# Optimization experiments

Hardware: AMD Instinct MI355X
Metric: run time of the kernel (lower is better)

## Reference

```python
import jax, jax.numpy as jnp
import numpy as np

P = 4  # polynomial kernel degree


def setup_inputs() -> dict:
    key = jax.random.key(0)
    k1, k2, k3, k4 = jax.random.split(key, 4)
    m, n, d = 16384, 8192, 64
    x_p = jax.random.normal(k1, (m, d), dtype=jnp.float32)
    X = jax.random.normal(k2, (n, d), dtype=jnp.float32)
    alpha = jax.random.uniform(k3, (n,), dtype=jnp.float32, minval=0.0, maxval=0.2)
    b = jax.random.uniform(k4, (1,), dtype=jnp.float32, minval=0.0, maxval=0.2)
    return {"x_p": x_p, "X": X, "alpha": alpha, "b": b}


def reference(x_p, X, alpha, b):
    # SVR prediction with polynomial kernel, vectorized:
    # f(x_p) = sum_i alpha_i * (1 + x_p . X_i)^P + b
    # x_p: [m, d], X: [n, d] -> K: [m, n]
    K = (1.0 + jnp.einsum('md,nd->mn', x_p, X)) ** P
    return K @ alpha + b  # [m]
```

## Files before the change

### kernel.cpp

```cpp
#include <hip/hip_runtime.h>
#include <hip/hip_bf16.h>
#include <stdint.h>


typedef __attribute__((ext_vector_type(8))) short bf16x8;
typedef __attribute__((ext_vector_type(8))) unsigned short ushort8;
typedef __attribute__((ext_vector_type(4))) float f32x4;

#define MM 16384
#define NN 8192
#define DD 64
#define NSPLIT 4
#define CHUNK 64
#define CHUNKS_PER_BLK 32
#define BM 128

__device__ __forceinline__ unsigned short f2bf(float f) {
    uint32_t u = __float_as_uint(f);
    uint32_t r = (u + 0x7FFFu + ((u >> 16) & 1u)) >> 16;
    return (unsigned short)r;
}

__device__ __forceinline__ void gll16(const void* g, void* l) {
    __builtin_amdgcn_global_load_lds(
        (const __attribute__((address_space(1))) unsigned int*)g,
        (__attribute__((address_space(3))) unsigned int*)l, 16, 0, 0);
}

__global__ void convert_kernel(const float* __restrict__ xp,
                               const float* __restrict__ X,
                               const float* __restrict__ alpha,
                               unsigned short* __restrict__ xbf,
                               unsigned short* __restrict__ Xs,
                               float* __restrict__ alpha4f) {
    const int xp4 = MM * DD / 4;
    const int xu = NN * DD / 8;
    const int tot = xp4 + xu;
    int tid0 = blockIdx.x * blockDim.x + threadIdx.x;
    if (tid0 < NN) alpha4f[tid0] = sqrtf(sqrtf(alpha[tid0]));
    int stride = gridDim.x * blockDim.x;
    for (int i = tid0; i < tot; i += stride) {
        if (i < xp4) {
            float4 v = ((const float4*)xp)[i];
            ushort4 o;
            o.x = f2bf(v.x); o.y = f2bf(v.y); o.z = f2bf(v.z); o.w = f2bf(v.w);
            *(ushort4*)(xbf + (size_t)i * 4) = o;
        } else {
            int u = i - xp4;
            int n = u >> 3;
            int slot = u & 7;
            float a4 = sqrtf(sqrtf(alpha[n]));
            float4 va = ((const float4*)X)[n * 16 + slot * 2];
            float4 vb = ((const float4*)X)[n * 16 + slot * 2 + 1];
            ushort8 o;
            o[0] = f2bf(va.x * a4); o[1] = f2bf(va.y * a4);
            o[2] = f2bf(va.z * a4); o[3] = f2bf(va.w * a4);
            o[4] = f2bf(vb.x * a4); o[5] = f2bf(vb.y * a4);
            o[6] = f2bf(vb.z * a4); o[7] = f2bf(vb.w * a4);
            size_t dst = (size_t)(n >> 6) * 4096 + (n & 63) * 64
                       + ((slot ^ (n & 7)) * 8);
            *(ushort8*)(Xs + dst) = o;
        }
    }
}

#define LOAD_B(bvar, bufp)                                            \
    {                                                                 \
        _Pragma("unroll")                                             \
        for (int nt = 0; nt < 4; ++nt) {                              \
            const int rr2 = nt * 16 + r;                              \
            const char* rowp = (bufp) + rr2 * 128;                    \
            _Pragma("unroll")                                         \
            for (int bh = 0; bh < 2; ++bh) {                          \
                const int slot = (bh * 4 + g) ^ (rr2 & 7);            \
                bvar[nt][bh] = *(const bf16x8*)(rowp + slot * 16);    \
            }                                                         \
        }                                                             \
    }

#define MFMA_SET(accv, bvar, avv)                                     \
    {                                                                 \
        _Pragma("unroll")                                             \
        for (int mt = 0; mt < 2; ++mt)                                \
            _Pragma("unroll")                                         \
            for (int nt = 0; nt < 4; ++nt)                            \
                accv[mt][nt] = (f32x4){avv[nt], avv[nt], avv[nt], avv[nt]}; \
        _Pragma("unroll")                                             \
        for (int bh = 0; bh < 2; ++bh)                                \
            _Pragma("unroll")                                         \
            for (int nt = 0; nt < 4; ++nt)                            \
                _Pragma("unroll")                                     \
                for (int mt = 0; mt < 2; ++mt)                        \
                    accv[mt][nt] = __builtin_amdgcn_mfma_f32_16x16x32_bf16( \
                        a[mt][bh], bvar[nt][bh], accv[mt][nt], 0, 0, 0);    \
    }

#define EPILOGUE(accv)                                                \
    {                                                                 \
        _Pragma("unroll")                                             \
        for (int mt = 0; mt < 2; ++mt)                                \
            _Pragma("unroll")                                         \
            for (int nt = 0; nt < 4; ++nt)                            \
                _Pragma("unroll")                                     \
                for (int i = 0; i < 4; ++i) {                         \
                    float t = accv[mt][nt][i];                        \
                    float t2 = t * t;                                 \
                    red[mt][i] = fmaf(t2, t2, red[mt][i]);            \
                }                                                     \
    }

#define STAGE(CLOC)                                                   \
    {                                                                 \
        const char* gs = (const char*)Xs                              \
            + (size_t)(chunk0 + (CLOC)) * 8192 + tid * 16;            \
        char* lb = smem + ((CLOC) & 3) * 8192 + w * 1024;             \
        gll16(gs, lb);                                                \
        gll16(gs + 4096, lb + 4096);                                  \
    }

#define PHASE(CLOC, ACC_THIS, ACC_PREV, DO_PREV)                      \
    {                                                                 \
        const int cst = ((CLOC) + 2 < CHUNKS_PER_BLK)                 \
                          ? (CLOC) + 2 : (CLOC) + 2 - CHUNKS_PER_BLK; \
        STAGE(cst);                                                   \
        const int cal = ((CLOC) + 1 < CHUNKS_PER_BLK) ? (CLOC) + 1 : 0; \
        float av_n[4];                                                \
        _Pragma("unroll")                                             \
        for (int nt = 0; nt < 4; ++nt)                                \
            av_n[nt] = alpha4f[(chunk0 + cal) * CHUNK + nt * 16 + r]; \
        asm volatile("s_waitcnt vmcnt(12)" ::: "memory");             \
        __builtin_amdgcn_s_barrier();                                 \
        __builtin_amdgcn_sched_barrier(0);                            \
        bf16x8 bfr[4][2];                                             \
        LOAD_B(bfr, smem + ((CLOC) & 3) * 8192);                      \
        MFMA_SET(ACC_THIS, bfr, av_c);                                \
        if (DO_PREV) EPILOGUE(ACC_PREV);                              \
        _Pragma("unroll")                                             \
        for (int nt = 0; nt < 4; ++nt) av_c[nt] = av_n[nt];           \
    }

__global__ __launch_bounds__(256) void svr_main(
        const unsigned short* __restrict__ xbf,
        const unsigned short* __restrict__ Xs,
        const float* __restrict__ alpha4f,
        float* __restrict__ partials) {
    __shared__ char smem[32768];
    const int tid  = threadIdx.x;
    const int lane = tid & 63;
    const int w    = tid >> 6;
    const int r    = lane & 15;
    const int g    = lane >> 4;
    const int mgroup = blockIdx.x >> 2;
    const int ns     = blockIdx.x & 3;

    bf16x8 a[2][2];
#pragma unroll
    for (int mt = 0; mt < 2; ++mt)
#pragma unroll
        for (int ks = 0; ks < 2; ++ks)
            a[mt][ks] = *(const bf16x8*)(
                xbf + (size_t)(mgroup * BM + w * 32 + mt * 16 + r) * DD
                    + ks * 32 + g * 8);

    f32x4 red[2];
#pragma unroll
    for (int mt = 0; mt < 2; ++mt) red[mt] = (f32x4){0.f, 0.f, 0.f, 0.f};

    const int chunk0 = ns * CHUNKS_PER_BLK;

    float av_c[4];
    STAGE(0);
#pragma unroll
    for (int nt = 0; nt < 4; ++nt)
        av_c[nt] = alpha4f[chunk0 * CHUNK + nt * 16 + r];
    STAGE(1);

    f32x4 accE[2][4], accO[2][4];

#pragma unroll 1
    for (int p = 0; p < CHUNKS_PER_BLK / 2; ++p) {
        PHASE(2 * p,     accE, accO, (p > 0));
        PHASE(2 * p + 1, accO, accE, true);
    }
    EPILOGUE(accO);

#pragma unroll
    for (int mt = 0; mt < 2; ++mt)
#pragma unroll
        for (int i = 0; i < 4; ++i) {
            float v = red[mt][i];
            v += __shfl_xor(v, 1);
            v += __shfl_xor(v, 2);
            v += __shfl_xor(v, 4);
            v += __shfl_xor(v, 8);
            red[mt][i] = v;
        }
    if (r == 0) {
#pragma unroll
        for (int mt = 0; mt < 2; ++mt)
#pragma unroll
            for (int i = 0; i < 4; ++i) {
                int row = mgroup * BM + w * 32 + mt * 16 + g * 4 + i;
                partials[(size_t)ns * MM + row] = red[mt][i];
            }
    }
}

__global__ void finalize_kernel(const float* __restrict__ partials,
                                const float* __restrict__ bbias,
                                float* __restrict__ out) {
    int m = blockIdx.x * blockDim.x + threadIdx.x;
    if (m < MM) {
        float s = bbias[0];
#pragma unroll
        for (int c = 0; c < NSPLIT; ++c) s += partials[(size_t)c * MM + m];
        out[m] = s;
    }
}

extern "C" void kernel_launch(void* const* d_in, const int* in_sizes, int n_in,
                              void* d_out, int out_size, void* d_ws, size_t ws_size,
                              hipStream_t stream) {
    const float* xp    = (const float*)d_in[0];
    const float* X     = (const float*)d_in[1];
    const float* alpha = (const float*)d_in[2];
    const float* b     = (const float*)d_in[3];
    float* out = (float*)d_out;

    unsigned short* xbf = (unsigned short*)d_ws;
    unsigned short* Xs  = xbf + (size_t)MM * DD;
    float* alpha4f = (float*)(Xs + (size_t)NN * DD);
    float* partials = alpha4f + NN;

    hipLaunchKernelGGL(convert_kernel, dim3(1280), dim3(256), 0, stream,
                       xp, X, alpha, xbf, Xs, alpha4f);

    hipLaunchKernelGGL(svr_main, dim3(128 * NSPLIT), dim3(256), 0, stream,
                       xbf, Xs, alpha4f, partials);

    hipLaunchKernelGGL(finalize_kernel, dim3(MM / 256), dim3(256), 0, stream,
                       partials, b, out);
}
```

Baseline: 35.72 us.

## Switch to 32x32x16 MFMA with double-buffered LDS and simpler sync

Replaces the 16x16x32 bf16 MFMA tiling with 32x32x16 MFMAs, so each wave computes a 32x64 tile using two 16-element accumulators and a new lane-to-row mapping in the final reduction. The four-deep LDS ring with prefetch distance two and an explicit vmcnt wait is replaced by a two-buffer scheme that prefetches one chunk ahead and calls __syncthreads at the end of each chunk. The larger MFMA shape cuts instruction count and LDS B-fragment reads per FLOP. The cost is a shallower prefetch and a full barrier every chunk, which may expose global-load latency.

```diff
diff --git a/kernel.cpp b/kernel.cpp
--- a/kernel.cpp
+++ b/kernel.cpp
@@ -5,7 +5,7 @@
 
 typedef __attribute__((ext_vector_type(8))) short bf16x8;
 typedef __attribute__((ext_vector_type(8))) unsigned short ushort8;
-typedef __attribute__((ext_vector_type(4))) float f32x4;
+typedef __attribute__((ext_vector_type(16))) float f32x16;
 
 #define MM 16384
 #define NN 8192
@@ -64,79 +64,61 @@
     }
 }
 
-#define LOAD_B(bvar, bufp)                                            \
-    {                                                                 \
-        _Pragma("unroll")                                             \
-        for (int nt = 0; nt < 4; ++nt) {                              \
-            const int rr2 = nt * 16 + r;                              \
-            const char* rowp = (bufp) + rr2 * 128;                    \
-            _Pragma("unroll")                                         \
-            for (int bh = 0; bh < 2; ++bh) {                          \
-                const int slot = (bh * 4 + g) ^ (rr2 & 7);            \
-                bvar[nt][bh] = *(const bf16x8*)(rowp + slot * 16);    \
-            }                                                         \
-        }                                                             \
-    }
-
-#define MFMA_SET(accv, bvar, avv)                                     \
-    {                                                                 \
-        _Pragma("unroll")                                             \
-        for (int mt = 0; mt < 2; ++mt)                                \
-            _Pragma("unroll")                                         \
-            for (int nt = 0; nt < 4; ++nt)                            \
-                accv[mt][nt] = (f32x4){avv[nt], avv[nt], avv[nt], avv[nt]}; \
-        _Pragma("unroll")                                             \
-        for (int bh = 0; bh < 2; ++bh)                                \
-            _Pragma("unroll")                                         \
-            for (int nt = 0; nt < 4; ++nt)                            \
-                _Pragma("unroll")                                     \
-                for (int mt = 0; mt < 2; ++mt)                        \
-                    accv[mt][nt] = __builtin_amdgcn_mfma_f32_16x16x32_bf16( \
-                        a[mt][bh], bvar[nt][bh], accv[mt][nt], 0, 0, 0);    \
-    }
-
-#define EPILOGUE(accv)                                                \
-    {                                                                 \
-        _Pragma("unroll")                                             \
-        for (int mt = 0; mt < 2; ++mt)                                \
-            _Pragma("unroll")                                         \
-            for (int nt = 0; nt < 4; ++nt)                            \
-                _Pragma("unroll")                                     \
-                for (int i = 0; i < 4; ++i) {                         \
-                    float t = accv[mt][nt][i];                        \
-                    float t2 = t * t;                                 \
-                    red[mt][i] = fmaf(t2, t2, red[mt][i]);            \
-                }                                                     \
-    }
-
 #define STAGE(CLOC)                                                   \
     {                                                                 \
         const char* gs = (const char*)Xs                              \
             + (size_t)(chunk0 + (CLOC)) * 8192 + tid * 16;            \
-        char* lb = smem + ((CLOC) & 3) * 8192 + w * 1024;             \
+        char* lb = smem + ((CLOC) & 1) * 8192 + w * 1024;             \
         gll16(gs, lb);                                                \
         gll16(gs + 4096, lb + 4096);                                  \
     }
 
-#define PHASE(CLOC, ACC_THIS, ACC_PREV, DO_PREV)                      \
+#define DO_CHUNK(CLOC, ACC_THIS, ACC_PREV, DOPREV)                    \
     {                                                                 \
-        const int cst = ((CLOC) + 2 < CHUNKS_PER_BLK)                 \
-                          ? (CLOC) + 2 : (CLOC) + 2 - CHUNKS_PER_BLK; \
-        STAGE(cst);                                                   \
-        const int cal = ((CLOC) + 1 < CHUNKS_PER_BLK) ? (CLOC) + 1 : 0; \
-        float av_n[4];                                                \
-        _Pragma("unroll")                                             \
-        for (int nt = 0; nt < 4; ++nt)                                \
-            av_n[nt] = alpha4f[(chunk0 + cal) * CHUNK + nt * 16 + r]; \
-        asm volatile("s_waitcnt vmcnt(12)" ::: "memory");             \
-        __builtin_amdgcn_s_barrier();                                 \
-        __builtin_amdgcn_sched_barrier(0);                            \
-        bf16x8 bfr[4][2];                                             \
-        LOAD_B(bfr, smem + ((CLOC) & 3) * 8192);                      \
-        MFMA_SET(ACC_THIS, bfr, av_c);                                \
-        if (DO_PREV) EPILOGUE(ACC_PREV);                              \
-        _Pragma("unroll")                                             \
-        for (int nt = 0; nt < 4; ++nt) av_c[nt] = av_n[nt];           \
+        float av_n[2];                                                \
+        if ((CLOC) + 1 < CHUNKS_PER_BLK) {                            \
+            STAGE((CLOC) + 1);                                        \
+            _Pragma("unroll")                                         \
+            for (int nt = 0; nt < 2; ++nt)                            \
+                av_n[nt] = alpha4f[(chunk0 + (CLOC) + 1) * CHUNK      \
+                                   + nt * 32 + nl];                   \
+        }                                                             \
+        const char* buf = smem + ((CLOC) & 1) * 8192;                 \
+        bf16x8 bfr[2][4];                                             \
+        _Pragma("unroll")                                             \
+        for (int nt = 0; nt < 2; ++nt) {                              \
+            const int n = nt * 32 + nl;                               \
+            const char* rowp = buf + n * 128;                         \
+            _Pragma("unroll")                                         \
+            for (int ks = 0; ks < 4; ++ks) {                          \
+                const int slot = (ks * 2 + kh) ^ (n & 7);             \
+                bfr[nt][ks] = *(const bf16x8*)(rowp + slot * 16);     \
+            }                                                         \
+        }                                                             \
+        _Pragma("unroll")                                             \
+        for (int nt = 0; nt < 2; ++nt) {                              \
+            _Pragma("unroll")                                         \
+            for (int i = 0; i < 16; ++i) ACC_THIS[nt][i] = av_c[nt];  \
+        }                                                             \
+        _Pragma("unroll")                                             \
+        for (int ks = 0; ks < 4; ++ks)                                \
+            _Pragma("unroll")                                         \
+            for (int nt = 0; nt < 2; ++nt)                            \
+                ACC_THIS[nt] = __builtin_amdgcn_mfma_f32_32x32x16_bf16( \
+                    a[ks], bfr[nt][ks], ACC_THIS[nt], 0, 0, 0);       \
+        if (DOPREV) {                                                 \
+            _Pragma("unroll")                                         \
+            for (int nt = 0; nt < 2; ++nt)                            \
+                _Pragma("unroll")                                     \
+                for (int i = 0; i < 16; ++i) {                        \
+                    float t = ACC_PREV[nt][i];                        \
+                    float t2 = t * t;                                 \
+                    red[i] = fmaf(t2, t2, red[i]);                    \
+                }                                                     \
+        }                                                             \
+        __syncthreads();                                              \
+        _Pragma("unroll")                                             \
+        for (int nt = 0; nt < 2; ++nt) av_c[nt] = av_n[nt];           \
     }
 
 __global__ __launch_bounds__(256) void svr_main(
@@ -144,65 +126,68 @@
         const unsigned short* __restrict__ Xs,
         const float* __restrict__ alpha4f,
         float* __restrict__ partials) {
-    __shared__ char smem[32768];
+    __shared__ char smem[16384];
     const int tid  = threadIdx.x;
     const int lane = tid & 63;
     const int w    = tid >> 6;
-    const int r    = lane & 15;
-    const int g    = lane >> 4;
+    const int nl   = lane & 31;
+    const int kh   = lane >> 5;
     const int mgroup = blockIdx.x >> 2;
     const int ns     = blockIdx.x & 3;
 
-    bf16x8 a[2][2];
-#pragma unroll
-    for (int mt = 0; mt < 2; ++mt)
-#pragma unroll
-        for (int ks = 0; ks < 2; ++ks)
-            a[mt][ks] = *(const bf16x8*)(
-                xbf + (size_t)(mgroup * BM + w * 32 + mt * 16 + r) * DD
-                    + ks * 32 + g * 8);
-
-    f32x4 red[2];
-#pragma unroll
-    for (int mt = 0; mt < 2; ++mt) red[mt] = (f32x4){0.f, 0.f, 0.f, 0.f};
+    bf16x8 a[4];
+#pragma unroll
+    for (int ks = 0; ks < 4; ++ks)
+        a[ks] = *(const bf16x8*)(
+            xbf + (size_t)(mgroup * BM + w * 32 + nl) * DD
+                + ks * 16 + kh * 8);
+
+    float red[16];
+#pragma unroll
+    for (int i = 0; i < 16; ++i) red[i] = 0.f;
 
     const int chunk0 = ns * CHUNKS_PER_BLK;
 
-    float av_c[4];
     STAGE(0);
-#pragma unroll
-    for (int nt = 0; nt < 4; ++nt)
-        av_c[nt] = alpha4f[chunk0 * CHUNK + nt * 16 + r];
-    STAGE(1);
-
-    f32x4 accE[2][4], accO[2][4];
+    float av_c[2];
+#pragma unroll
+    for (int nt = 0; nt < 2; ++nt)
+        av_c[nt] = alpha4f[chunk0 * CHUNK + nt * 32 + nl];
+    __syncthreads();
+
+    f32x16 accE[2], accO[2];
 
 #pragma unroll 1
     for (int p = 0; p < CHUNKS_PER_BLK / 2; ++p) {
-        PHASE(2 * p,     accE, accO, (p > 0));
-        PHASE(2 * p + 1, accO, accE, true);
-    }
-    EPILOGUE(accO);
-
-#pragma unroll
-    for (int mt = 0; mt < 2; ++mt)
-#pragma unroll
-        for (int i = 0; i < 4; ++i) {
-            float v = red[mt][i];
-            v += __shfl_xor(v, 1);
-            v += __shfl_xor(v, 2);
-            v += __shfl_xor(v, 4);
-            v += __shfl_xor(v, 8);
-            red[mt][i] = v;
+        DO_CHUNK(2 * p,     accE, accO, (p > 0));
+        DO_CHUNK(2 * p + 1, accO, accE, true);
+    }
+#pragma unroll
+    for (int nt = 0; nt < 2; ++nt)
+#pragma unroll
+        for (int i = 0; i < 16; ++i) {
+            float t = accO[nt][i];
+            float t2 = t * t;
+            red[i] = fmaf(t2, t2, red[i]);
         }
-    if (r == 0) {
-#pragma unroll
-        for (int mt = 0; mt < 2; ++mt)
-#pragma unroll
-            for (int i = 0; i < 4; ++i) {
-                int row = mgroup * BM + w * 32 + mt * 16 + g * 4 + i;
-                partials[(size_t)ns * MM + row] = red[mt][i];
-            }
+
+#pragma unroll
+    for (int i = 0; i < 16; ++i) {
+        float v = red[i];
+        v += __shfl_xor(v, 1);
+        v += __shfl_xor(v, 2);
+        v += __shfl_xor(v, 4);
+        v += __shfl_xor(v, 8);
+        v += __shfl_xor(v, 16);
+        red[i] = v;
+    }
+    if (nl == 0) {
+#pragma unroll
+        for (int i = 0; i < 16; ++i) {
+            int row_local = (i & 3) + 8 * (i >> 2) + 4 * kh;
+            int row = mgroup * BM + w * 32 + row_local;
+            partials[(size_t)ns * MM + row] = red[i];
+        }
     }
 }
 
```

New measurement: 36.80 us. +3.0%, slower.
